# Optimization experiments

Measured on AMD Instinct MI355X. Metric: run time of the kernel, lower is better.

## Reference

```python
import jax, jax.numpy as jnp
import numpy as np

N = 131072        # total points
M = 34            # max_num_neighbors (hard-coded in forward)
K = 15            # kernel points (torch-points3d default for 3D KPConv)
C_IN, C_OUT = 32, 64
POINT_INFLUENCE = 0.04        # prev_grid_size * sigma
KERNEL_RADIUS = 1.5 * POINT_INFLUENCE  # _INFLUENCE_TO_RADIUS * point_influence
BN_EPS = 1e-5
NEG_SLOPE = 0.2


def setup_inputs() -> dict:
    key = jax.random.key(0)
    ks = jax.random.split(key, 6)
    # points in a [0, 0.1]^3 box so random neighbors can fall inside the influence radius
    xyz = jax.random.uniform(ks[0], (N, 3), jnp.float32) * 0.1
    feats = jax.random.normal(ks[1], (N, C_IN), jnp.float32)
    neighbor_idx = jax.random.randint(ks[2], (N, M), 0, N, dtype=jnp.int32)
    # fixed kernel-point disposition: points inside a sphere of radius KERNEL_RADIUS
    kp_dir = jax.random.normal(ks[3], (K, 3), jnp.float32)
    kp_dir = kp_dir / jnp.linalg.norm(kp_dir, axis=1, keepdims=True)
    kp_rad = jax.random.uniform(ks[4], (K, 1), jnp.float32) ** (1.0 / 3.0)
    k_points = kp_dir * kp_rad * KERNEL_RADIUS
    weight = jax.random.normal(ks[5], (K, C_IN, C_OUT), jnp.float32) / np.sqrt(K * C_IN)
    gamma = jnp.ones((C_OUT,), jnp.float32)
    beta = jnp.zeros((C_OUT,), jnp.float32)
    return {"xyz": xyz, "feats": feats, "neighbor_idx": neighbor_idx,
            "weight": weight, "k_points": k_points, "gamma": gamma, "beta": beta}


def _kpconv(xyz, feats, neighbor_idx, weight, k_points):
    # shadow point / shadow feature row for out-of-range neighbor index == N
    sup = jnp.concatenate([xyz, jnp.full((1, 3), 1e6, xyz.dtype)], axis=0)
    f = jnp.concatenate([feats, jnp.zeros((1, feats.shape[1]), feats.dtype)], axis=0)
    # [N, M, 3] neighbor offsets relative to each query point
    nb = sup[neighbor_idx] - xyz[:, None, :]
    # [N, M, K] distance from each neighbor to each kernel point
    diff = nb[:, :, None, :] - k_points[None, None, :, :]
    dist = jnp.sqrt(jnp.sum(diff * diff, axis=-1))
    # linear kernel influence, 'sum' aggregation
    w = jnp.maximum(0.0, 1.0 - dist / POINT_INFLUENCE)          # [N, M, K]
    nb_f = f[neighbor_idx]                                       # [N, M, C_IN]
    wf = jnp.einsum('nmk,nmc->nkc', w, nb_f)                     # [N, K, C_IN]
    return jnp.einsum('nkc,kcd->nd', wf, weight)                 # [N, C_OUT]


def reference(xyz, feats, neighbor_idx, weight, k_points, gamma, beta):
    out = _kpconv(xyz, feats, neighbor_idx, weight, k_points)
    # FastBatchNorm1d (training-mode batch statistics) + LeakyReLU(0.2)
    mean = jnp.mean(out, axis=0)
    var = jnp.mean((out - mean) ** 2, axis=0)
    out = (out - mean) * jax.lax.rsqrt(var + BN_EPS) * gamma + beta
    return jnp.where(out >= 0, out, NEG_SLOPE * out)
```

## Files before the change

### kernel.cpp

```cpp
#include <hip/hip_runtime.h>

#define NPTS 131072
#define MNBR 34
#define KP 15
#define CIN 32
#define COUT 64
#define INV_INFL 25.0f
#define BN_EPS 1e-5f
#define NEG_SLOPE 0.2f
#define PPB 32
#define NBLK (NPTS / PPB)
#define RS 20

typedef unsigned short u16;
typedef unsigned int u32;
typedef short short8 __attribute__((ext_vector_type(8)));
typedef float f32x4 __attribute__((ext_vector_type(4)));

static __device__ __forceinline__ u16 f2bf(float f) {
    u32 x = __float_as_uint(f);
    x += 0x7fffu + ((x >> 16) & 1u);
    return (u16)(x >> 16);
}
static __device__ __forceinline__ u32 pk2bf(float lo, float hi) {
    u32 a = __float_as_uint(lo) + 0x8000u;
    u32 b = __float_as_uint(hi) + 0x8000u;
    return (a >> 16) | (b & 0xffff0000u);
}

#define WS_WT   0u
#define WS_SCSH 65536u
#define WS_SP   131072u
#define WS_QP   1179648u
#define WS_FB   2228224u

__global__ __launch_bounds__(256) void prep(const float* __restrict__ Wg,
                                            const float* __restrict__ feats,
                                            u16* __restrict__ WT, u32* __restrict__ FBu) {
    int b = blockIdx.x;
    if (b < 120) {
        int tid2 = b * 256 + threadIdx.x;
        int i = tid2 >> 6, d = tid2 & 63;
        WT[d * 480 + i] = f2bf(Wg[tid2]);
    } else {
        int g = (b - 120) * 256 + threadIdx.x;
        if (g < ((NPTS + 1) * CIN) / 2) {
            int e = g * 2;
            u32 v = 0;
            if (e < NPTS * CIN)
                v = (u32)f2bf(feats[e]) | ((u32)f2bf(feats[e + 1]) << 16);
            FBu[g] = v;
        }
    }
}

__global__ __launch_bounds__(256) void kpconv_conv(
    const float* __restrict__ xyz, const int* __restrict__ nbr,
    const u16* __restrict__ FB, const u16* __restrict__ WT,
    const float* __restrict__ kpts, float* __restrict__ out,
    float* __restrict__ Sp, float* __restrict__ Qp)
{
    __shared__ u32 wf[PPB * 256];
    __shared__ u32 nbf[4][64 * RS];
    __shared__ u16 wk[4][16 * 64];

    const int tid = threadIdx.x, lane = tid & 63, wave = tid >> 6;
    const int q = lane >> 4, t = lane & 15;

    float kx[16], ky[16], kz[16];
    #pragma unroll
    for (int k = 0; k < KP; ++k) {
        kx[k] = kpts[3 * k]; ky[k] = kpts[3 * k + 1]; kz[k] = kpts[3 * k + 2];
    }
    kx[15] = 1e6f; ky[15] = 1e6f; kz[15] = 1e6f;

    u32* nb = nbf[wave];
    u16* wl = wk[wave];

    for (int p = 0; p < 8; ++p) {
        const int row = wave * 8 + p;
        const int n = blockIdx.x * PPB + row;
        const float qx = xyz[3 * n], qy = xyz[3 * n + 1], qz = xyz[3 * n + 2];

        int ii = NPTS;
        if (lane < MNBR) ii = nbr[n * MNBR + lane];
        if ((unsigned)ii > (unsigned)NPTS) ii = NPTS;
        const int il = ii < NPTS ? ii : 0;
        float ox = xyz[3 * il] - qx, oy = xyz[3 * il + 1] - qy, oz = xyz[3 * il + 2] - qz;
        if (ii >= NPTS) { ox = 1e6f; oy = 0.f; oz = 0.f; }

        const uint4* fr = (const uint4*)(FB + (size_t)ii * CIN);
        uint4 f0 = fr[0], f1 = fr[1], f2 = fr[2], f3 = fr[3];
        uint4* nrow = (uint4*)(nb + lane * RS);
        nrow[0] = f0; nrow[1] = f1; nrow[2] = f2; nrow[3] = f3;

        #pragma unroll
        for (int k = 0; k < 16; ++k) {
            float dx = ox - kx[k], dy = oy - ky[k], dz = oz - kz[k];
            float d = __builtin_amdgcn_sqrtf(fmaf(dx, dx, fmaf(dy, dy, dz * dz)));
            float w = fmaxf(0.f, fmaf(d, -INV_INFL, 1.f));
            int unit = (lane >> 3) ^ (k & 7);
            wl[k * 64 + unit * 8 + (lane & 7)] = (u16)((__float_as_uint(w) + 0x8000u) >> 16);
        }
        __asm__ volatile("s_waitcnt lgkmcnt(0)" ::: "memory");

        short8 a0 = *(const short8*)&wl[t * 64 + (((0 * 4 + q) ^ (t & 7)) << 3)];
        short8 a1 = *(const short8*)&wl[t * 64 + (((1 * 4 + q) ^ (t & 7)) << 3)];

        u32 r0[8], r1[8];
        #pragma unroll
        for (int j = 0; j < 8; ++j) {
            r0[j] = nb[(8 * q + j) * RS + t];
            r1[j] = nb[(8 * q + j + 32) * RS + t];
        }
        union { short8 v; u32 d[4]; } e0, o0, e1, o1;
        #pragma unroll
        for (int i2 = 0; i2 < 4; ++i2) {
            u32 a = r0[2 * i2], b = r0[2 * i2 + 1];
            e0.d[i2] = (a & 0xffffu) | (b << 16);
            o0.d[i2] = (a >> 16) | (b & 0xffff0000u);
            a = r1[2 * i2]; b = r1[2 * i2 + 1];
            e1.d[i2] = (a & 0xffffu) | (b << 16);
            o1.d[i2] = (a >> 16) | (b & 0xffff0000u);
        }

        f32x4 c0 = {0.f, 0.f, 0.f, 0.f}, c1 = {0.f, 0.f, 0.f, 0.f};
        c0 = __builtin_amdgcn_mfma_f32_16x16x32_bf16(a0, e0.v, c0, 0, 0, 0);
        c0 = __builtin_amdgcn_mfma_f32_16x16x32_bf16(a1, e1.v, c0, 0, 0, 0);
        c1 = __builtin_amdgcn_mfma_f32_16x16x32_bf16(a0, o0.v, c1, 0, 0, 0);
        c1 = __builtin_amdgcn_mfma_f32_16x16x32_bf16(a1, o1.v, c1, 0, 0, 0);

        #pragma unroll
        for (int r = 0; r < 4; ++r) {
            int ko = q * 4 + r;
            u32 pk = pk2bf(c0[r], c1[r]);
            int unit = ko * 4 + (t >> 2);
            wf[row * 256 + ((unit ^ (row & 7)) << 2) + (t & 3)] = pk;
        }
        __asm__ volatile("s_waitcnt lgkmcnt(0)" ::: "memory");
    }
    __syncthreads();

    const int wcol = wave * 16 + t;
    f32x4 acc0 = {0.f, 0.f, 0.f, 0.f}, acc1 = {0.f, 0.f, 0.f, 0.f};
    const u16* wtp = WT + wcol * 480 + q * 8;
    const int row0 = t, row1 = 16 + t;
    #pragma unroll
    for (int ks = 0; ks < KP; ++ks) {
        short8 b = *(const short8*)(wtp + ks * 32);
        const int u = ks * 4 + q;
        short8 a0 = *(const short8*)&wf[row0 * 256 + ((u ^ (row0 & 7)) << 2)];
        short8 a1 = *(const short8*)&wf[row1 * 256 + ((u ^ (row1 & 7)) << 2)];
        acc0 = __builtin_amdgcn_mfma_f32_16x16x32_bf16(a0, b, acc0, 0, 0, 0);
        acc1 = __builtin_amdgcn_mfma_f32_16x16x32_bf16(a1, b, acc1, 0, 0, 0);
    }
    const int base = blockIdx.x * PPB;
    float s = 0.f, q2 = 0.f;
    #pragma unroll
    for (int r = 0; r < 4; ++r) {
        float v0 = acc0[r], v1 = acc1[r];
        out[(base +      q * 4 + r) * COUT + wcol] = v0;
        out[(base + 16 + q * 4 + r) * COUT + wcol] = v1;
        s += v0 + v1;
        q2 = fmaf(v0, v0, q2); q2 = fmaf(v1, v1, q2);
    }
    s  += __shfl_xor(s, 16, 64);  s  += __shfl_xor(s, 32, 64);
    q2 += __shfl_xor(q2, 16, 64); q2 += __shfl_xor(q2, 32, 64);
    if (q == 0) {
        Sp[wcol * NBLK + blockIdx.x] = s;
        Qp[wcol * NBLK + blockIdx.x] = q2;
    }
}

__global__ __launch_bounds__(256) void bn_reduce(
    const float* __restrict__ Sp, const float* __restrict__ Qp,
    const float* __restrict__ gamma, const float* __restrict__ beta,
    float* __restrict__ scsh)
{
    const int ch = blockIdx.x;
    const float4* S4 = (const float4*)(Sp + ch * NBLK);
    const float4* Q4 = (const float4*)(Qp + ch * NBLK);
    float s = 0.f, qq = 0.f;
    #pragma unroll
    for (int r = 0; r < NBLK / 4 / 256; ++r) {
        float4 a = S4[threadIdx.x + 256 * r]; s  += a.x + a.y + a.z + a.w;
        float4 b = Q4[threadIdx.x + 256 * r]; qq += b.x + b.y + b.z + b.w;
    }
    #pragma unroll
    for (int off = 1; off < 64; off <<= 1) {
        s += __shfl_xor(s, off, 64); qq += __shfl_xor(qq, off, 64);
    }
    __shared__ float red[8];
    const int w = threadIdx.x >> 6;
    if ((threadIdx.x & 63) == 0) { red[w * 2] = s; red[w * 2 + 1] = qq; }
    __syncthreads();
    if (threadIdx.x == 0) {
        s  = red[0] + red[2] + red[4] + red[6];
        qq = red[1] + red[3] + red[5] + red[7];
        float mean = s * (1.0f / NPTS);
        float var  = qq * (1.0f / NPTS) - mean * mean;
        float sc = gamma[ch] * rsqrtf(var + BN_EPS);
        scsh[ch] = sc;
        scsh[64 + ch] = beta[ch] - mean * sc;
    }
}

__global__ __launch_bounds__(256) void bn_apply(
    float* __restrict__ out, const float* __restrict__ scsh)
{
    __shared__ float sc[64], sh[64];
    const int tid = threadIdx.x;
    if (tid < 64) { sc[tid] = scsh[tid]; sh[tid] = scsh[64 + tid]; }
    __syncthreads();
    const int gid = blockIdx.x * 256 + tid;
    float4 v = ((const float4*)out)[gid];
    const int c0 = (gid * 4) & 63;
    float y0 = fmaf(v.x, sc[c0 + 0], sh[c0 + 0]);
    float y1 = fmaf(v.y, sc[c0 + 1], sh[c0 + 1]);
    float y2 = fmaf(v.z, sc[c0 + 2], sh[c0 + 2]);
    float y3 = fmaf(v.w, sc[c0 + 3], sh[c0 + 3]);
    float4 w;
    w.x = fmaxf(y0, NEG_SLOPE * y0);
    w.y = fmaxf(y1, NEG_SLOPE * y1);
    w.z = fmaxf(y2, NEG_SLOPE * y2);
    w.w = fmaxf(y3, NEG_SLOPE * y3);
    ((float4*)out)[gid] = w;
}

extern "C" void kernel_launch(void* const* d_in, const int* in_sizes, int n_in,
                              void* d_out, int out_size, void* d_ws, size_t ws_size,
                              hipStream_t stream) {
    (void)in_sizes; (void)n_in; (void)out_size; (void)ws_size;
    const float* xyz   = (const float*)d_in[0];
    const float* feats = (const float*)d_in[1];
    const int*   nbr   = (const int*)d_in[2];
    const float* Wg    = (const float*)d_in[3];
    const float* kpts  = (const float*)d_in[4];
    const float* gamma = (const float*)d_in[5];
    const float* beta  = (const float*)d_in[6];
    float* out = (float*)d_out;
    char* ws = (char*)d_ws;
    u16*   WT   = (u16*)(ws + WS_WT);
    float* scsh = (float*)(ws + WS_SCSH);
    float* Sp   = (float*)(ws + WS_SP);
    float* Qp   = (float*)(ws + WS_QP);
    u16*   FB   = (u16*)(ws + WS_FB);

    prep<<<dim3(120 + 8193), dim3(256), 0, stream>>>(Wg, feats, WT, (u32*)FB);
    kpconv_conv<<<dim3(NBLK), dim3(256), 0, stream>>>(xyz, nbr, FB, WT, kpts, out, Sp, Qp);
    bn_reduce<<<dim3(64), dim3(256), 0, stream>>>(Sp, Qp, gamma, beta, scsh);
    bn_apply<<<dim3((NPTS * COUT) / (256 * 4)), dim3(256), 0, stream>>>(out, scsh);
}
```

Measured before the change: 237.3 us.

## Prefetch neighbor gathers across points and shrink blocks to 16 points with atomic BN bins

The conv kernel now processes 16 points per 128-thread block and software-pipelines neighbor index loads two points ahead and the gathered features and coordinates one point ahead in registers. This is meant to hide gather latency behind the weight computation. The distance computation is expanded algebraically using precomputed -2k and |k|^2 terms. The neighbor-feature LDS tile is transposed so it can be read with vector loads, and per-block BN partial sums are atomically accumulated into 2048 bins that prep zeroes. The changes raise register pressure and add atomics and an extra zeroing pass in exchange for better latency hiding.

```diff
diff --git a/kernel.cpp b/kernel.cpp
--- a/kernel.cpp
+++ b/kernel.cpp
@@ -8,9 +8,9 @@
 #define INV_INFL 25.0f
 #define BN_EPS 1e-5f
 #define NEG_SLOPE 0.2f
-#define PPB 32
+#define PPB 16
 #define NBLK (NPTS / PPB)
-#define RS 20
+#define NBIN 2048
 
 typedef unsigned short u16;
 typedef unsigned int u32;
@@ -31,18 +31,19 @@
 #define WS_WT   0u
 #define WS_SCSH 65536u
 #define WS_SP   131072u
-#define WS_QP   1179648u
-#define WS_FB   2228224u
+#define WS_QP   655360u
+#define WS_FB   1179648u
 
 __global__ __launch_bounds__(256) void prep(const float* __restrict__ Wg,
                                             const float* __restrict__ feats,
-                                            u16* __restrict__ WT, u32* __restrict__ FBu) {
+                                            u16* __restrict__ WT, u32* __restrict__ FBu,
+                                            float* __restrict__ SpQp) {
     int b = blockIdx.x;
     if (b < 120) {
         int tid2 = b * 256 + threadIdx.x;
         int i = tid2 >> 6, d = tid2 & 63;
         WT[d * 480 + i] = f2bf(Wg[tid2]);
-    } else {
+    } else if (b < 120 + 8193) {
         int g = (b - 120) * 256 + threadIdx.x;
         if (g < ((NPTS + 1) * CIN) / 2) {
             int e = g * 2;
@@ -51,77 +52,112 @@
                 v = (u32)f2bf(feats[e]) | ((u32)f2bf(feats[e + 1]) << 16);
             FBu[g] = v;
         }
-    }
-}
-
-__global__ __launch_bounds__(256) void kpconv_conv(
+    } else {
+        int idx = (b - 8313) * 256 + threadIdx.x;
+        if (idx < 2 * 64 * NBIN) SpQp[idx] = 0.f;
+    }
+}
+
+__global__ __launch_bounds__(128, 3) void kpconv_conv(
     const float* __restrict__ xyz, const int* __restrict__ nbr,
     const u16* __restrict__ FB, const u16* __restrict__ WT,
     const float* __restrict__ kpts, float* __restrict__ out,
     float* __restrict__ Sp, float* __restrict__ Qp)
 {
     __shared__ u32 wf[PPB * 256];
-    __shared__ u32 nbf[4][64 * RS];
-    __shared__ u16 wk[4][16 * 64];
+    __shared__ u32 nbt[2][16 * 68];
+    __shared__ u16 wk[2][16 * 64];
 
     const int tid = threadIdx.x, lane = tid & 63, wave = tid >> 6;
     const int q = lane >> 4, t = lane & 15;
 
-    float kx[16], ky[16], kz[16];
+    float ax[16], ay[16], az[16], ck[16];
     #pragma unroll
     for (int k = 0; k < KP; ++k) {
-        kx[k] = kpts[3 * k]; ky[k] = kpts[3 * k + 1]; kz[k] = kpts[3 * k + 2];
-    }
-    kx[15] = 1e6f; ky[15] = 1e6f; kz[15] = 1e6f;
-
-    u32* nb = nbf[wave];
+        float kx = kpts[3 * k], ky = kpts[3 * k + 1], kz = kpts[3 * k + 2];
+        ax[k] = -2.f * kx; ay[k] = -2.f * ky; az[k] = -2.f * kz;
+        ck[k] = fmaf(kx, kx, fmaf(ky, ky, kz * kz));
+    }
+    ax[15] = 0.f; ay[15] = 0.f; az[15] = 0.f; ck[15] = 1e12f;
+
+    u32* nb = nbt[wave];
     u16* wl = wk[wave];
+    const int pbase = blockIdx.x * PPB + wave * 8;
+
+    int ci = NPTS;
+    if (lane < MNBR) ci = nbr[(size_t)pbase * MNBR + lane];
+    if ((unsigned)ci > (unsigned)NPTS) ci = NPTS;
+    int nn = NPTS;
+    if (lane < MNBR) nn = nbr[(size_t)(pbase + 1) * MNBR + lane];
+    if ((unsigned)nn > (unsigned)NPTS) nn = NPTS;
+
+    int il = ci < NPTS ? ci : 0;
+    float cnx = xyz[3 * il], cny = xyz[3 * il + 1], cnz = xyz[3 * il + 2];
+    const uint4* fr = (const uint4*)(FB + (size_t)ci * CIN);
+    uint4 cf0 = fr[0], cf1 = fr[1], cf2 = fr[2], cf3 = fr[3];
 
     for (int p = 0; p < 8; ++p) {
-        const int row = wave * 8 + p;
-        const int n = blockIdx.x * PPB + row;
+        int nn2 = NPTS;
+        if (p < 6) {
+            if (lane < MNBR) nn2 = nbr[(size_t)(pbase + p + 2) * MNBR + lane];
+            if ((unsigned)nn2 > (unsigned)NPTS) nn2 = NPTS;
+        }
+        float nx1 = 0.f, ny1 = 0.f, nz1 = 0.f;
+        uint4 nf0 = {}, nf1 = {}, nf2 = {}, nf3 = {};
+        if (p < 7) {
+            int il1 = nn < NPTS ? nn : 0;
+            nx1 = xyz[3 * il1]; ny1 = xyz[3 * il1 + 1]; nz1 = xyz[3 * il1 + 2];
+            const uint4* fr1 = (const uint4*)(FB + (size_t)nn * CIN);
+            nf0 = fr1[0]; nf1 = fr1[1]; nf2 = fr1[2]; nf3 = fr1[3];
+        }
+
+        const int n = pbase + p;
         const float qx = xyz[3 * n], qy = xyz[3 * n + 1], qz = xyz[3 * n + 2];
-
-        int ii = NPTS;
-        if (lane < MNBR) ii = nbr[n * MNBR + lane];
-        if ((unsigned)ii > (unsigned)NPTS) ii = NPTS;
-        const int il = ii < NPTS ? ii : 0;
-        float ox = xyz[3 * il] - qx, oy = xyz[3 * il + 1] - qy, oz = xyz[3 * il + 2] - qz;
-        if (ii >= NPTS) { ox = 1e6f; oy = 0.f; oz = 0.f; }
-
-        const uint4* fr = (const uint4*)(FB + (size_t)ii * CIN);
-        uint4 f0 = fr[0], f1 = fr[1], f2 = fr[2], f3 = fr[3];
-        uint4* nrow = (uint4*)(nb + lane * RS);
-        nrow[0] = f0; nrow[1] = f1; nrow[2] = f2; nrow[3] = f3;
+        float ox = cnx - qx, oy = cny - qy, oz = cnz - qz;
+        if (ci >= NPTS) { ox = 1e6f; oy = 0.f; oz = 0.f; }
+        const float oo = fmaf(ox, ox, fmaf(oy, oy, oz * oz));
 
         #pragma unroll
         for (int k = 0; k < 16; ++k) {
-            float dx = ox - kx[k], dy = oy - ky[k], dz = oz - kz[k];
-            float d = __builtin_amdgcn_sqrtf(fmaf(dx, dx, fmaf(dy, dy, dz * dz)));
+            float d2 = fmaf(ox, ax[k], fmaf(oy, ay[k], fmaf(oz, az[k], ck[k]))) + oo;
+            float d = __builtin_amdgcn_sqrtf(d2);
             float w = fmaxf(0.f, fmaf(d, -INV_INFL, 1.f));
-            int unit = (lane >> 3) ^ (k & 7);
-            wl[k * 64 + unit * 8 + (lane & 7)] = (u16)((__float_as_uint(w) + 0x8000u) >> 16);
-        }
-        __asm__ volatile("s_waitcnt lgkmcnt(0)" ::: "memory");
-
-        short8 a0 = *(const short8*)&wl[t * 64 + (((0 * 4 + q) ^ (t & 7)) << 3)];
-        short8 a1 = *(const short8*)&wl[t * 64 + (((1 * 4 + q) ^ (t & 7)) << 3)];
-
-        u32 r0[8], r1[8];
-        #pragma unroll
-        for (int j = 0; j < 8; ++j) {
-            r0[j] = nb[(8 * q + j) * RS + t];
-            r1[j] = nb[(8 * q + j + 32) * RS + t];
-        }
+            wl[k * 64 + ((((lane >> 3) ^ (k & 7))) << 3) + (lane & 7)] =
+                (u16)((__float_as_uint(w) + 0x8000u) >> 16);
+        }
+
+        {
+            u32 fd[16] = {cf0.x, cf0.y, cf0.z, cf0.w, cf1.x, cf1.y, cf1.z, cf1.w,
+                          cf2.x, cf2.y, cf2.z, cf2.w, cf3.x, cf3.y, cf3.z, cf3.w};
+            #pragma unroll
+            for (int w16 = 0; w16 < 16; ++w16)
+                nb[w16 * 68 + lane] = fd[w16];
+        }
+
+        cnx = nx1; cny = ny1; cnz = nz1;
+        cf0 = nf0; cf1 = nf1; cf2 = nf2; cf3 = nf3;
+        ci = nn; nn = nn2;
+
+        short8 a0 = *(const short8*)&wl[t * 64 + (((q) ^ (t & 7)) << 3)];
+        short8 a1 = *(const short8*)&wl[t * 64 + (((4 + q) ^ (t & 7)) << 3)];
+
+        uint4 b0 = *(const uint4*)&nb[t * 68 + 8 * q];
+        uint4 b1 = *(const uint4*)&nb[t * 68 + 8 * q + 4];
+        uint4 b2 = *(const uint4*)&nb[t * 68 + 8 * q + 32];
+        uint4 b3 = *(const uint4*)&nb[t * 68 + 8 * q + 36];
         union { short8 v; u32 d[4]; } e0, o0, e1, o1;
-        #pragma unroll
-        for (int i2 = 0; i2 < 4; ++i2) {
-            u32 a = r0[2 * i2], b = r0[2 * i2 + 1];
-            e0.d[i2] = (a & 0xffffu) | (b << 16);
-            o0.d[i2] = (a >> 16) | (b & 0xffff0000u);
-            a = r1[2 * i2]; b = r1[2 * i2 + 1];
-            e1.d[i2] = (a & 0xffffu) | (b << 16);
-            o1.d[i2] = (a >> 16) | (b & 0xffff0000u);
+        {
+            u32 r0[8] = {b0.x, b0.y, b0.z, b0.w, b1.x, b1.y, b1.z, b1.w};
+            u32 r1[8] = {b2.x, b2.y, b2.z, b2.w, b3.x, b3.y, b3.z, b3.w};
+            #pragma unroll
+            for (int i2 = 0; i2 < 4; ++i2) {
+                u32 a = r0[2 * i2], b = r0[2 * i2 + 1];
+                e0.d[i2] = (a & 0xffffu) | (b << 16);
+                o0.d[i2] = (a >> 16) | (b & 0xffff0000u);
+                a = r1[2 * i2]; b = r1[2 * i2 + 1];
+                e1.d[i2] = (a & 0xffffu) | (b << 16);
+                o1.d[i2] = (a >> 16) | (b & 0xffff0000u);
+            }
         }
 
         f32x4 c0 = {0.f, 0.f, 0.f, 0.f}, c1 = {0.f, 0.f, 0.f, 0.f};
@@ -130,6 +166,7 @@
         c1 = __builtin_amdgcn_mfma_f32_16x16x32_bf16(a0, o0.v, c1, 0, 0, 0);
         c1 = __builtin_amdgcn_mfma_f32_16x16x32_bf16(a1, o1.v, c1, 0, 0, 0);
 
+        const int row = wave * 8 + p;
         #pragma unroll
         for (int r = 0; r < 4; ++r) {
             int ko = q * 4 + r;
@@ -137,38 +174,43 @@
             int unit = ko * 4 + (t >> 2);
             wf[row * 256 + ((unit ^ (row & 7)) << 2) + (t & 3)] = pk;
         }
-        __asm__ volatile("s_waitcnt lgkmcnt(0)" ::: "memory");
     }
     __syncthreads();
 
-    const int wcol = wave * 16 + t;
-    f32x4 acc0 = {0.f, 0.f, 0.f, 0.f}, acc1 = {0.f, 0.f, 0.f, 0.f};
-    const u16* wtp = WT + wcol * 480 + q * 8;
-    const int row0 = t, row1 = 16 + t;
+    const int wcol0 = (wave * 2 + 0) * 16 + t;
+    const int wcol1 = (wave * 2 + 1) * 16 + t;
+    f32x4 A0 = {0.f, 0.f, 0.f, 0.f}, A1 = {0.f, 0.f, 0.f, 0.f};
+    const u16* wt0 = WT + wcol0 * 480 + q * 8;
+    const u16* wt1 = WT + wcol1 * 480 + q * 8;
     #pragma unroll
     for (int ks = 0; ks < KP; ++ks) {
-        short8 b = *(const short8*)(wtp + ks * 32);
         const int u = ks * 4 + q;
-        short8 a0 = *(const short8*)&wf[row0 * 256 + ((u ^ (row0 & 7)) << 2)];
-        short8 a1 = *(const short8*)&wf[row1 * 256 + ((u ^ (row1 & 7)) << 2)];
-        acc0 = __builtin_amdgcn_mfma_f32_16x16x32_bf16(a0, b, acc0, 0, 0, 0);
-        acc1 = __builtin_amdgcn_mfma_f32_16x16x32_bf16(a1, b, acc1, 0, 0, 0);
+        short8 a  = *(const short8*)&wf[t * 256 + ((u ^ (t & 7)) << 2)];
+        short8 bb0 = *(const short8*)(wt0 + ks * 32);
+        short8 bb1 = *(const short8*)(wt1 + ks * 32);
+        A0 = __builtin_amdgcn_mfma_f32_16x16x32_bf16(a, bb0, A0, 0, 0, 0);
+        A1 = __builtin_amdgcn_mfma_f32_16x16x32_bf16(a, bb1, A1, 0, 0, 0);
     }
     const int base = blockIdx.x * PPB;
-    float s = 0.f, q2 = 0.f;
+    float s0 = 0.f, q0 = 0.f, s1 = 0.f, q1 = 0.f;
     #pragma unroll
     for (int r = 0; r < 4; ++r) {
-        float v0 = acc0[r], v1 = acc1[r];
-        out[(base +      q * 4 + r) * COUT + wcol] = v0;
-        out[(base + 16 + q * 4 + r) * COUT + wcol] = v1;
-        s += v0 + v1;
-        q2 = fmaf(v0, v0, q2); q2 = fmaf(v1, v1, q2);
-    }
-    s  += __shfl_xor(s, 16, 64);  s  += __shfl_xor(s, 32, 64);
-    q2 += __shfl_xor(q2, 16, 64); q2 += __shfl_xor(q2, 32, 64);
+        float v0 = A0[r], v1 = A1[r];
+        out[(base + q * 4 + r) * COUT + wcol0] = v0;
+        out[(base + q * 4 + r) * COUT + wcol1] = v1;
+        s0 += v0; q0 = fmaf(v0, v0, q0);
+        s1 += v1; q1 = fmaf(v1, v1, q1);
+    }
+    s0 += __shfl_xor(s0, 16, 64); s0 += __shfl_xor(s0, 32, 64);
+    q0 += __shfl_xor(q0, 16, 64); q0 += __shfl_xor(q0, 32, 64);
+    s1 += __shfl_xor(s1, 16, 64); s1 += __shfl_xor(s1, 32, 64);
+    q1 += __shfl_xor(q1, 16, 64); q1 += __shfl_xor(q1, 32, 64);
     if (q == 0) {
-        Sp[wcol * NBLK + blockIdx.x] = s;
-        Qp[wcol * NBLK + blockIdx.x] = q2;
+        const int bin = blockIdx.x >> 2;
+        atomicAdd(&Sp[wcol0 * NBIN + bin], s0);
+        atomicAdd(&Qp[wcol0 * NBIN + bin], q0);
+        atomicAdd(&Sp[wcol1 * NBIN + bin], s1);
+        atomicAdd(&Qp[wcol1 * NBIN + bin], q1);
     }
 }
 
@@ -178,11 +220,11 @@
     float* __restrict__ scsh)
 {
     const int ch = blockIdx.x;
-    const float4* S4 = (const float4*)(Sp + ch * NBLK);
-    const float4* Q4 = (const float4*)(Qp + ch * NBLK);
+    const float4* S4 = (const float4*)(Sp + ch * NBIN);
+    const float4* Q4 = (const float4*)(Qp + ch * NBIN);
     float s = 0.f, qq = 0.f;
     #pragma unroll
-    for (int r = 0; r < NBLK / 4 / 256; ++r) {
+    for (int r = 0; r < NBIN / 4 / 256; ++r) {
         float4 a = S4[threadIdx.x + 256 * r]; s  += a.x + a.y + a.z + a.w;
         float4 b = Q4[threadIdx.x + 256 * r]; qq += b.x + b.y + b.z + b.w;
     }
@@ -246,8 +288,8 @@
     float* Qp   = (float*)(ws + WS_QP);
     u16*   FB   = (u16*)(ws + WS_FB);
 
-    prep<<<dim3(120 + 8193), dim3(256), 0, stream>>>(Wg, feats, WT, (u32*)FB);
-    kpconv_conv<<<dim3(NBLK), dim3(256), 0, stream>>>(xyz, nbr, FB, WT, kpts, out, Sp, Qp);
+    prep<<<dim3(120 + 8193 + 1024), dim3(256), 0, stream>>>(Wg, feats, WT, (u32*)FB, Sp);
+    kpconv_conv<<<dim3(NBLK), dim3(128), 0, stream>>>(xyz, nbr, FB, WT, kpts, out, Sp, Qp);
     bn_reduce<<<dim3(64), dim3(256), 0, stream>>>(Sp, Qp, gamma, beta, scsh);
     bn_apply<<<dim3((NPTS * COUT) / (256 * 4)), dim3(256), 0, stream>>>(out, scsh);
 }
```

Measured after the change: 248.0 us. 1.04x slower.
